# Optimization experiments

Hardware: AMD Instinct MI355X
Metric: run time of the kernel (lower is better)

Reference implementation:

```python
import jax, jax.numpy as jnp
import numpy as np

FEATS_DIM = 2048
NUM_CLASSES = 20
R_EASY, R_HARD = 5, 20
M_SMALL, M_BIG = 3, 6   # cfg.m, cfg.M (morphology structure widths)
N_HEADS = 4
B, T = 16, 750


def conv1d(x, w, b=None, pad=0):
    # x: [B, Cin, T], w: [Cout, Cin, K]
    out = jax.lax.conv_general_dilated(x, w, (1,), [(pad, pad)],
                                       dimension_numbers=('NCH', 'OIH', 'NCH'))
    return out if b is None else out + b[None, :, None]


def leaky(x):
    return jnp.where(x >= 0, x, 0.2 * x)


def mha(q, k, v, in_w, in_b, out_w, out_b):
    # torch nn.MultiheadAttention (batch_first, eval-mode: dropout off)
    Bq, Lq, E = q.shape
    Lk = k.shape[1]
    d = E // N_HEADS
    wq, wk, wv = jnp.split(in_w, 3, axis=0)
    bq, bk, bv = jnp.split(in_b, 3)
    qh = (q @ wq.T + bq).reshape(Bq, Lq, N_HEADS, d).transpose(0, 2, 1, 3)
    kh = (k @ wk.T + bk).reshape(Bq, Lk, N_HEADS, d).transpose(0, 2, 1, 3)
    vh = (v @ wv.T + bv).reshape(Bq, Lk, N_HEADS, d).transpose(0, 2, 1, 3)
    scores = jnp.einsum('bhqd,bhkd->bhqk', qh, kh) / jnp.sqrt(jnp.float32(d))
    attn = jax.nn.softmax(scores, axis=-1)
    o = jnp.einsum('bhqk,bhkd->bhqd', attn, vh).transpose(0, 2, 1, 3).reshape(Bq, Lq, E)
    return o @ out_w.T + out_b


def relational_head(x, P):
    # x: [B, 74, 2048] (the double transpose in the torch code cancels out)
    in1, in2 = x[:, :37], x[:, 37:]
    ao2 = mha(in1, in2, in2, P['in_w'], P['in_b'], P['out_w'], P['out_b'])
    ao1 = mha(in2, in1, in1, P['in_w'], P['in_b'], P['out_w'], P['out_b'])
    y = jnp.swapaxes(jnp.concatenate([ao1, ao2], axis=1), -1, -2)   # [B,2048,74]
    y = leaky(conv1d(y, P['c1_w'], P['c1_b'], pad=1))               # [B,128,74]
    y = leaky(conv1d(y, P['c2_w'], P['c2_b'], pad=1))               # [B,32,74]
    y = leaky(y @ P['l1_w'].T + P['l1_b'])                          # [B,32,10]
    y = y.reshape(y.shape[0], -1)                                   # [B,320]
    return jax.nn.sigmoid(y @ P['l2_w'].T + P['l2_b'])              # [B,1]


def select_topk(scores, emb, k):
    idx = jnp.argsort(-scores, axis=1)[:, :k]                       # descending
    return jnp.take_along_axis(emb, idx[:, :, None], axis=1)


def _morph(b, M, erosion):
    # scipy binary_erosion/dilation with structure ones((1,M)), border_value=0.
    # erosion: offsets [-M//2, M-1-M//2]; dilation (reflected): [-(M-1-M//2), M//2].
    Tn = b.shape[1]
    lo, hi = (M // 2, M - 1 - M // 2) if erosion else (M - 1 - M // 2, M // 2)
    pad = jnp.pad(b, ((0, 0), (lo, hi)))
    s = jnp.stack([pad[:, j:j + Tn] for j in range(M)], axis=0)
    return jnp.min(s, axis=0) if erosion else jnp.max(s, axis=0)


def cola_forward(x, P):
    # train=True path, eval-mode dropout (deterministic identity)
    Bn, Tn, _ = x.shape
    k_easy, k_hard = Tn // R_EASY, Tn // R_HARD
    feat = jnp.swapaxes(x, -1, -2)                                   # [B,2048,T]
    emb_c = jax.nn.relu(conv1d(feat, P['w_embed'], P['b_embed'], pad=1))
    embeddings = jnp.swapaxes(emb_c, -1, -2)                         # [B,T,2048]
    cas = jnp.swapaxes(jax.nn.relu(conv1d(emb_c, P['w_cls'], None)), -1, -2)  # [B,T,C]
    actionness = cas.sum(axis=-1)                                    # [B,T]
    a2 = jax.nn.relu(conv1d(actionness[:, None, :], P['tf1_w'], P['tf1_b'], pad=1))
    a2 = jax.nn.relu(conv1d(a2, P['tf2_w'], P['tf2_b'], pad=1))[:, 0]
    # easy snippet mining
    act_rev = actionness.max(axis=1, keepdims=True) - actionness
    easy_act = select_topk(actionness, embeddings, k_easy)
    easy_bkg = select_topk(act_rev, embeddings, k_easy)
    # hard snippet mining (binary morphology; indices are non-differentiable)
    a_det = jax.lax.stop_gradient(actionness)
    med = jnp.median(a_det, axis=1, keepdims=True)
    abin = jnp.where(a_det > med, 1.0, 0.0)
    inner = _morph(abin, M_SMALL, True) - _morph(abin, M_BIG, True)
    outer = _morph(abin, M_BIG, False) - _morph(abin, M_SMALL, False)
    hard_act = select_topk(actionness * inner, embeddings, k_hard)
    hard_bkg = select_topk(actionness * outer, embeddings, k_hard)
    split = lambda y: (y[:, :37], y[:, 37:74], y[:, 74:111], y[:, 111:148])
    ea0, ea1, ea2, ea3 = split(easy_act)
    eb0, eb1, eb2, eb3 = split(easy_bkg)
    rh = lambda a, b: relational_head(jnp.concatenate([a, b], axis=1), P)
    re_a_02 = rh(ea3, ea2); re_a_03 = rh(ea0, ea3); re_a_0h = rh(ea1, hard_act)
    re_b_02 = rh(eb3, eb2); re_b_03 = rh(eb0, eb3); re_b_0h = rh(eb1, hard_bkg)
    re_ab_23 = rh(ea2, eb3); re_ab_32 = rh(eb2, ea3); re_ab_33 = rh(ea3, eb3)
    re_ab_h3 = rh(hard_act, eb3); re_ab_3h = rh(ea3, hard_bkg); re_ab_hh = rh(hard_bkg, hard_act)
    video_scores = jax.nn.softmax((-jnp.sort(-cas, axis=1))[:, :k_easy].mean(axis=1), axis=1)
    return (video_scores, actionness, a2, cas,
            re_a_0h, re_a_02, re_a_03, re_b_0h, re_b_02, re_b_03,
            re_ab_hh, re_ab_3h, re_ab_h3, re_ab_33, re_ab_32, re_ab_23,
            easy_act, easy_bkg, hard_act, hard_bkg)


PARAM_NAMES = ['w_embed', 'b_embed', 'w_cls', 'tf1_w', 'tf1_b', 'tf2_w', 'tf2_b',
               'in_w', 'in_b', 'out_w', 'out_b', 'c1_w', 'c1_b', 'c2_w', 'c2_b',
               'l1_w', 'l1_b', 'l2_w', 'l2_b']


def setup_inputs() -> dict:
    key = jax.random.key(0)
    ks = jax.random.split(key, 20)
    sc = 0.02
    inp = {
        'x': jax.random.normal(ks[0], (B, T, FEATS_DIM), jnp.float32),
        'w_embed': sc * jax.random.normal(ks[1], (2048, FEATS_DIM, 3), jnp.float32),
        'b_embed': sc * jax.random.normal(ks[2], (2048,), jnp.float32),
        'w_cls': sc * jax.random.normal(ks[3], (NUM_CLASSES, 2048, 1), jnp.float32),
        'tf1_w': sc * jax.random.normal(ks[4], (1, 1, 3), jnp.float32),
        'tf1_b': sc * jax.random.normal(ks[5], (1,), jnp.float32),
        'tf2_w': sc * jax.random.normal(ks[6], (1, 1, 3), jnp.float32),
        'tf2_b': sc * jax.random.normal(ks[7], (1,), jnp.float32),
        'in_w': sc * jax.random.normal(ks[8], (3 * 2048, 2048), jnp.float32),
        'in_b': sc * jax.random.normal(ks[9], (3 * 2048,), jnp.float32),
        'out_w': sc * jax.random.normal(ks[10], (2048, 2048), jnp.float32),
        'out_b': sc * jax.random.normal(ks[11], (2048,), jnp.float32),
        'c1_w': sc * jax.random.normal(ks[12], (128, 2048, 3), jnp.float32),
        'c1_b': sc * jax.random.normal(ks[13], (128,), jnp.float32),
        'c2_w': sc * jax.random.normal(ks[14], (32, 128, 3), jnp.float32),
        'c2_b': sc * jax.random.normal(ks[15], (32,), jnp.float32),
        'l1_w': sc * jax.random.normal(ks[16], (10, 74), jnp.float32),
        'l1_b': sc * jax.random.normal(ks[17], (10,), jnp.float32),
        'l2_w': sc * jax.random.normal(ks[18], (1, 10 * 32), jnp.float32),
        'l2_b': sc * jax.random.normal(ks[19], (1,), jnp.float32),
    }
    return inp


def reference(x, w_embed, b_embed, w_cls, tf1_w, tf1_b, tf2_w, tf2_b,
              in_w, in_b, out_w, out_b, c1_w, c1_b, c2_w, c2_b,
              l1_w, l1_b, l2_w, l2_b):
    P = dict(w_embed=w_embed, b_embed=b_embed, w_cls=w_cls, tf1_w=tf1_w, tf1_b=tf1_b,
             tf2_w=tf2_w, tf2_b=tf2_b, in_w=in_w, in_b=in_b, out_w=out_w, out_b=out_b,
             c1_w=c1_w, c1_b=c1_b, c2_w=c2_w, c2_b=c2_b,
             l1_w=l1_w, l1_b=l1_b, l2_w=l2_w, l2_b=l2_b)
    return cola_forward(x, P)
```

## Files before the change

kernel.cpp:

```cpp
#include <hip/hip_runtime.h>


static __device__ __forceinline__ float leaky_f(float x) { return x >= 0.f ? x : 0.2f * x; }

typedef _Float16 f16;
typedef f16 f16x4 __attribute__((ext_vector_type(4)));
typedef f16 f16x8 __attribute__((ext_vector_type(8)));
typedef float f32x4 __attribute__((ext_vector_type(4)));

__device__ __constant__ int PIDX[12][2] = {
  {1, 8}, {3, 2}, {0, 3}, {5, 9}, {7, 6}, {4, 7},
  {9, 8}, {3, 9}, {8, 7}, {3, 7}, {6, 3}, {2, 7}};

__global__ __launch_bounds__(256) void pack_w_k(const float* __restrict__ src,
                                                float* __restrict__ dst,
                                                int N, int KC, int taps) {
  long total = (long)N * KC * taps;
  long i = (long)blockIdx.x * 256 + threadIdx.x;
  if (i >= total) return;
  long nk = (long)N * KC;
  int tap = (int)(i / nk);
  long rem = i - (long)tap * nk;
  int n = (int)(rem / KC);
  int k = (int)(rem - (long)n * KC);
  dst[i] = src[((long)n * KC + k) * taps + tap];
}

__global__ __launch_bounds__(256) void pack_frag_w_k(const float* __restrict__ src,
                                                     f16* __restrict__ dst,
                                                     int N, int KC, int taps) {
  int KCd32 = KC >> 5, gN = N >> 4;
  long total = (long)taps * KCd32 * gN * 512;
  long i = (long)blockIdx.x * 256 + threadIdx.x;
  if (i >= total) return;
  int e = (int)(i & 7);
  int lane = (int)((i >> 3) & 63);
  long rem = i >> 9;
  int g = (int)(rem % gN); rem /= gN;
  int kc = (int)(rem % KCd32);
  int tap = (int)(rem / KCd32);
  int n = g * 16 + (lane & 15);
  int k = kc * 32 + (lane >> 4) * 8 + e;
  float v = src[((long)n * KC + k) * taps + tap];
  f16 h = (f16)v;
  long f = ((long)tap * KCd32 + kc) * gN + g;
  dst[f * 1024 + lane * 8 + e] = h;
  dst[f * 1024 + 512 + lane * 8 + e] = (f16)(v - (float)h);
}

__global__ __launch_bounds__(256) void gemmf3_k(
    const float* __restrict__ A, const f16* __restrict__ Bf,
    const float* __restrict__ bias, float* __restrict__ C,
    int M, int N, int KC, int taps, int shift_base, int a_grp,
    int mblocks, int swz, int act) {
  __shared__ f16 Ah[128][40];
  __shared__ f16 Al[128][40];
  int t = threadIdx.x;
  int NB = gridDim.x;
  int linear = blockIdx.x;
  int wg = swz ? ((linear & 7) * (NB >> 3) + (linear >> 3)) : linear;
  int n0 = (wg / mblocks) * 128, m0 = (wg % mblocks) * 128;

  int sr = t >> 1;
  int sc = (t & 1) << 4;
  int am = m0 + sr;
  int ar = am % a_grp;

  int lane = t & 63, wv = t >> 6;
  int wm = (wv >> 1) * 64, wn = (wv & 1) * 64;
  int fr = lane & 15, fg = lane >> 4;

  int KCd32 = KC >> 5, gN = N >> 4;
  int g0 = ((n0 + wn) >> 4);

  f32x4 acc[4][4];
#pragma unroll
  for (int i = 0; i < 4; ++i)
#pragma unroll
    for (int j = 0; j < 4; ++j) acc[i][j] = (f32x4)(0.f);

  for (int tap = 0; tap < taps; ++tap) {
    int rr = ar + tap + shift_base;
    bool av = (am < M) && (rr >= 0) && (rr < a_grp);
    const float* ap = A + (long)(am + tap + shift_base) * KC + sc;
    long fb = ((long)tap * KCd32) * gN;
#pragma unroll 1
    for (int kc = 0; kc < KCd32; ++kc) {
      const f16* fp = Bf + (fb + (long)kc * gN + g0) * 1024 + lane * 8;
      f16x8 fbh[4], fbl[4];
#pragma unroll
      for (int j = 0; j < 4; ++j) {
        fbh[j] = *(const f16x8*)(fp + (long)j * 1024);
        fbl[j] = *(const f16x8*)(fp + (long)j * 1024 + 512);
      }
      float4 a4[4];
#pragma unroll
      for (int q = 0; q < 4; ++q)
        a4[q] = av ? *(const float4*)(ap + kc * 32 + q * 4)
                   : make_float4(0.f, 0.f, 0.f, 0.f);

      __syncthreads();
#pragma unroll
      for (int q = 0; q < 4; ++q) {
        float xs[4] = {a4[q].x, a4[q].y, a4[q].z, a4[q].w};
        f16x4 h4, l4;
#pragma unroll
        for (int e = 0; e < 4; ++e) {
          f16 hh = (f16)xs[e];
          h4[e] = hh;
          l4[e] = (f16)(xs[e] - (float)hh);
        }
        *(f16x4*)&Ah[sr][sc + q * 4] = h4;
        *(f16x4*)&Al[sr][sc + q * 4] = l4;
      }
      __syncthreads();

      f16x8 fah[4], fal[4];
#pragma unroll
      for (int i = 0; i < 4; ++i) {
        fah[i] = *(const f16x8*)&Ah[wm + i * 16 + fr][fg * 8];
        fal[i] = *(const f16x8*)&Al[wm + i * 16 + fr][fg * 8];
      }
#pragma unroll
      for (int i = 0; i < 4; ++i)
#pragma unroll
        for (int j = 0; j < 4; ++j) {
          acc[i][j] = __builtin_amdgcn_mfma_f32_16x16x32_f16(fal[i], fbh[j], acc[i][j], 0, 0, 0);
          acc[i][j] = __builtin_amdgcn_mfma_f32_16x16x32_f16(fah[i], fbl[j], acc[i][j], 0, 0, 0);
          acc[i][j] = __builtin_amdgcn_mfma_f32_16x16x32_f16(fah[i], fbh[j], acc[i][j], 0, 0, 0);
        }
    }
  }

#pragma unroll
  for (int i = 0; i < 4; ++i) {
#pragma unroll
    for (int j = 0; j < 4; ++j) {
      int col = n0 + wn + j * 16 + fr;
      if (col >= N) continue;
      float bb = bias ? bias[col] : 0.f;
#pragma unroll
      for (int r = 0; r < 4; ++r) {
        int m = m0 + wm + i * 16 + fg * 4 + r;
        if (m >= M) continue;
        float v = acc[i][j][r] + bb;
        if (act == 1) v = fmaxf(v, 0.f);
        else if (act == 2) v = leaky_f(v);
        C[(long)m * N + col] = v;
      }
    }
  }
}

template <int DACC>
__global__ __launch_bounds__(256) void gemm32_k(
    const float* __restrict__ A, const float* __restrict__ Bw,
    const float* __restrict__ bias, float* __restrict__ C,
    int M, int N, int KC, int taps, int shift_base,
    int a_grp, long a_bstride, int c_grp, long c_bstride, int act) {
  __shared__ __align__(16) float As[32][36];
  __shared__ __align__(16) float Bs[32][36];
  int tid = threadIdx.x;
  int n0 = blockIdx.x * 32, m0 = blockIdx.y * 32;
  int tx = tid & 15, ty = tid >> 4;
  int row_l = tid >> 3;
  int kq = (tid & 7) << 2;
  float accf[2][2] = {{0.f}};
  double accd[2][2];
  if (DACC) { accd[0][0] = accd[0][1] = accd[1][0] = accd[1][1] = 0.0; }
  int tpt = KC >> 5;
  int nkt = tpt * taps;
  int am = m0 + row_l;
  int agrp = 0, ar = 0;
  if (am < M) { agrp = am / a_grp; ar = am - agrp * a_grp; }
  int bn = n0 + row_l;
  for (int kt = 0; kt < nkt; ++kt) {
    int tap = kt / tpt;
    int k0 = (kt - tap * tpt) << 5;
    float4 av = make_float4(0.f, 0.f, 0.f, 0.f);
    float4 bv = make_float4(0.f, 0.f, 0.f, 0.f);
    if (am < M) {
      int rr = ar + tap + shift_base;
      if (rr >= 0 && rr < a_grp)
        av = *(const float4*)(A + (long)agrp * a_bstride + (long)rr * KC + (k0 + kq));
    }
    if (bn < N)
      bv = *(const float4*)(Bw + ((long)tap * N + bn) * KC + (k0 + kq));
    __syncthreads();
    As[kq + 0][row_l] = av.x; As[kq + 1][row_l] = av.y;
    As[kq + 2][row_l] = av.z; As[kq + 3][row_l] = av.w;
    Bs[kq + 0][row_l] = bv.x; Bs[kq + 1][row_l] = bv.y;
    Bs[kq + 2][row_l] = bv.z; Bs[kq + 3][row_l] = bv.w;
    __syncthreads();
    float tile[2][2] = {{0.f, 0.f}, {0.f, 0.f}};
#pragma unroll
    for (int k = 0; k < 32; ++k) {
      float2 a2 = *(const float2*)&As[k][ty << 1];
      float2 b2 = *(const float2*)&Bs[k][tx << 1];
      if (DACC) {
        tile[0][0] = fmaf(a2.x, b2.x, tile[0][0]);
        tile[0][1] = fmaf(a2.x, b2.y, tile[0][1]);
        tile[1][0] = fmaf(a2.y, b2.x, tile[1][0]);
        tile[1][1] = fmaf(a2.y, b2.y, tile[1][1]);
      } else {
        accf[0][0] = fmaf(a2.x, b2.x, accf[0][0]);
        accf[0][1] = fmaf(a2.x, b2.y, accf[0][1]);
        accf[1][0] = fmaf(a2.y, b2.x, accf[1][0]);
        accf[1][1] = fmaf(a2.y, b2.y, accf[1][1]);
      }
    }
    if (DACC) {
      accd[0][0] += (double)tile[0][0]; accd[0][1] += (double)tile[0][1];
      accd[1][0] += (double)tile[1][0]; accd[1][1] += (double)tile[1][1];
    }
  }
#pragma unroll
  for (int i = 0; i < 2; ++i) {
    int m = m0 + (ty << 1) + i;
    if (m >= M) continue;
    int grp = m / c_grp, r = m - grp * c_grp;
    float* crow = C + (long)grp * c_bstride + (long)r * N;
#pragma unroll
    for (int j = 0; j < 2; ++j) {
      int n = n0 + (tx << 1) + j;
      if (n >= N) continue;
      float v = DACC ? (float)accd[i][j] : accf[i][j];
      if (bias) v += bias[n];
      if (act == 1) v = fmaxf(v, 0.f);
      else if (act == 2) v = leaky_f(v);
      crow[n] = v;
    }
  }
}

template <int AMODE>
__global__ __launch_bounds__(256) void gemmx3_k(
    const float* __restrict__ Abase, const float* __restrict__ Bw,
    const float* __restrict__ bias, float* __restrict__ C,
    int M, int N, int K,
    long oEA, long oEB, long oHA, long oHB) {
  __shared__ _Float16 Ah[128][40];
  __shared__ _Float16 Al[128][40];
  __shared__ _Float16 Bh[128][40];
  __shared__ _Float16 Bl[128][40];
  int t = threadIdx.x;
  int m0 = blockIdx.y * 128, n0 = blockIdx.x * 128;

  int lr = t >> 3;
  int lq = t & 7;
  const float* arow[4];
  const float* brow[4];
#pragma unroll
  for (int p = 0; p < 4; ++p) {
    int m = m0 + p * 32 + lr;
    if (m < M) {
      if (AMODE == 0) {
        arow[p] = Abase + (long)m * K;
      } else {
        int inp = m / 592;
        int rem = m - inp * 592;
        int b = rem / 37;
        int r = rem - b * 37;
        long base, bstr;
        if (inp < 8) { base = (inp < 4 ? oEA : oEB) + (long)(inp & 3) * (37L * 2048); bstr = 150L * 2048; }
        else         { base = (inp == 8) ? oHA : oHB; bstr = 37L * 2048; }
        arow[p] = Abase + base + (long)b * bstr + (long)r * 2048;
      }
    } else arow[p] = nullptr;
    int n = n0 + p * 32 + lr;
    brow[p] = (n < N) ? (Bw + (long)n * K) : nullptr;
  }

  int lane = t & 63;
  int wv = t >> 6;
  int wm = (wv >> 1) * 64, wn = (wv & 1) * 64;
  int fr = lane & 15, fg = lane >> 4;

  f32x4 acc[4][4];
#pragma unroll
  for (int i = 0; i < 4; ++i)
#pragma unroll
    for (int j = 0; j < 4; ++j) acc[i][j] = (f32x4)(0.f);

  int nkt = K >> 5;
  for (int kt = 0; kt < nkt; ++kt) {
    int k0 = kt << 5;
    float4 av[4], bv[4];
#pragma unroll
    for (int p = 0; p < 4; ++p) {
      av[p] = arow[p] ? *(const float4*)(arow[p] + k0 + lq * 4) : make_float4(0.f, 0.f, 0.f, 0.f);
      bv[p] = brow[p] ? *(const float4*)(brow[p] + k0 + lq * 4) : make_float4(0.f, 0.f, 0.f, 0.f);
    }
    __syncthreads();
#pragma unroll
    for (int p = 0; p < 4; ++p) {
      int row = p * 32 + lr;
      float xs[4] = {av[p].x, av[p].y, av[p].z, av[p].w};
      f16x4 h, l;
#pragma unroll
      for (int e = 0; e < 4; ++e) {
        f16 hh = (f16)xs[e];
        h[e] = hh;
        l[e] = (f16)(xs[e] - (float)hh);
      }
      *(f16x4*)&Ah[row][lq * 4] = h;
      *(f16x4*)&Al[row][lq * 4] = l;
      float ys[4] = {bv[p].x, bv[p].y, bv[p].z, bv[p].w};
#pragma unroll
      for (int e = 0; e < 4; ++e) {
        f16 hh = (f16)ys[e];
        h[e] = hh;
        l[e] = (f16)(ys[e] - (float)hh);
      }
      *(f16x4*)&Bh[row][lq * 4] = h;
      *(f16x4*)&Bl[row][lq * 4] = l;
    }
    __syncthreads();
    f16x8 ah[4], alo[4], bh[4], blo[4];
#pragma unroll
    for (int i = 0; i < 4; ++i) {
      ah[i]  = *(const f16x8*)&Ah[wm + i * 16 + fr][fg * 8];
      alo[i] = *(const f16x8*)&Al[wm + i * 16 + fr][fg * 8];
      bh[i]  = *(const f16x8*)&Bh[wn + i * 16 + fr][fg * 8];
      blo[i] = *(const f16x8*)&Bl[wn + i * 16 + fr][fg * 8];
    }
#pragma unroll
    for (int i = 0; i < 4; ++i)
#pragma unroll
      for (int j = 0; j < 4; ++j) {
        acc[i][j] = __builtin_amdgcn_mfma_f32_16x16x32_f16(alo[i], bh[j], acc[i][j], 0, 0, 0);
        acc[i][j] = __builtin_amdgcn_mfma_f32_16x16x32_f16(ah[i], blo[j], acc[i][j], 0, 0, 0);
        acc[i][j] = __builtin_amdgcn_mfma_f32_16x16x32_f16(ah[i], bh[j], acc[i][j], 0, 0, 0);
      }
  }

#pragma unroll
  for (int i = 0; i < 4; ++i) {
#pragma unroll
    for (int j = 0; j < 4; ++j) {
      int col = n0 + wn + j * 16 + fr;
      if (col >= N) continue;
      float bb = bias ? bias[col] : 0.f;
#pragma unroll
      for (int r = 0; r < 4; ++r) {
        int m = m0 + wm + i * 16 + fg * 4 + r;
        if (m >= M) continue;
        C[(long)m * N + col] = acc[i][j][r] + bb;
      }
    }
  }
}

__global__ __launch_bounds__(256) void actionness_k(const float* __restrict__ cas,
                                                    float* __restrict__ act) {
  int p = blockIdx.x * 256 + threadIdx.x;
  if (p >= 16 * 750) return;
  double s = 0.0;
#pragma unroll
  for (int c = 0; c < 20; ++c) s += (double)cas[(long)p * 20 + c];
  act[p] = (float)s;
}

__global__ __launch_bounds__(256) void a2_k(const float* __restrict__ act,
                                            const float* __restrict__ tf1w, const float* __restrict__ tf1b,
                                            const float* __restrict__ tf2w, const float* __restrict__ tf2b,
                                            float* __restrict__ a2out) {
  __shared__ float s0[752];
  __shared__ float s1[752];
  int b = blockIdx.x, tid = threadIdx.x;
  for (int i = tid; i < 752; i += 256) { s0[i] = 0.f; s1[i] = 0.f; }
  __syncthreads();
  for (int t = tid; t < 750; t += 256) s0[t + 1] = act[b * 750 + t];
  __syncthreads();
  float w0 = tf1w[0], w1 = tf1w[1], w2 = tf1w[2], bb1 = tf1b[0];
  for (int t = tid; t < 750; t += 256)
    s1[t + 1] = fmaxf(w0 * s0[t] + w1 * s0[t + 1] + w2 * s0[t + 2] + bb1, 0.f);
  __syncthreads();
  float u0 = tf2w[0], u1 = tf2w[1], u2 = tf2w[2], bb2 = tf2b[0];
  for (int t = tid; t < 750; t += 256)
    a2out[b * 750 + t] = fmaxf(u0 * s1[t] + u1 * s1[t + 1] + u2 * s1[t + 2] + bb2, 0.f);
}

__global__ __launch_bounds__(256) void sort_topk_k(const float* __restrict__ scores,
                                                   int* __restrict__ out_idx, int K,
                                                   float* __restrict__ out_med,
                                                   float* __restrict__ out_mx) {
  __shared__ unsigned long long keys[1024];
  int b = blockIdx.x, tid = threadIdx.x;
  for (int i = tid; i < 1024; i += 256) {
    unsigned long long kv = 0ull;
    if (i < 750) {
      unsigned int bits = __float_as_uint(scores[b * 750 + i]);
      kv = ((unsigned long long)bits << 32) | (unsigned long long)(0xFFFFFFFFu - (unsigned)i);
    }
    keys[i] = kv;
  }
  __syncthreads();
  for (int k = 2; k <= 1024; k <<= 1) {
    for (int j = k >> 1; j > 0; j >>= 1) {
      for (int i = tid; i < 1024; i += 256) {
        int ixj = i ^ j;
        if (ixj > i) {
          unsigned long long a = keys[i], c = keys[ixj];
          bool sw = ((i & k) == 0) ? (a < c) : (a > c);
          if (sw) { keys[i] = c; keys[ixj] = a; }
        }
      }
      __syncthreads();
    }
  }
  for (int i = tid; i < K; i += 256)
    out_idx[b * K + i] = (int)(0xFFFFFFFFu - (unsigned int)(keys[i] & 0xFFFFFFFFull));
  if (tid == 0) {
    if (out_mx) out_mx[b] = __uint_as_float((unsigned int)(keys[0] >> 32));
    if (out_med) {
      float v1 = __uint_as_float((unsigned int)(keys[374] >> 32));
      float v2 = __uint_as_float((unsigned int)(keys[375] >> 32));
      out_med[b] = 0.5f * (v1 + v2);
    }
  }
}

__global__ __launch_bounds__(256) void morph_k(const float* __restrict__ act,
                                               const float* __restrict__ med,
                                               const float* __restrict__ mxv,
                                               float* __restrict__ arev,
                                               float* __restrict__ hsa,
                                               float* __restrict__ hsb) {
  __shared__ float ab[756];
  int b = blockIdx.x, tid = threadIdx.x;
  float m = med[b], M = mxv[b];
  for (int i = tid; i < 756; i += 256) ab[i] = 0.f;
  __syncthreads();
  for (int t = tid; t < 750; t += 256) {
    float a = act[b * 750 + t];
    ab[t + 3] = (a > m) ? 1.f : 0.f;
    arev[b * 750 + t] = M - a;
  }
  __syncthreads();
  for (int t = tid; t < 750; t += 256) {
    float e3 = fminf(ab[t + 2], fminf(ab[t + 3], ab[t + 4]));
    float e6 = fminf(fminf(ab[t], ab[t + 1]),
                     fminf(fminf(ab[t + 2], ab[t + 3]), fminf(ab[t + 4], ab[t + 5])));
    float d3 = fmaxf(ab[t + 2], fmaxf(ab[t + 3], ab[t + 4]));
    float d6 = fmaxf(fmaxf(ab[t + 1], ab[t + 2]),
                     fmaxf(fmaxf(ab[t + 3], ab[t + 4]), fmaxf(ab[t + 5], ab[t + 6])));
    float a = act[b * 750 + t];
    hsa[b * 750 + t] = a * (e3 - e6);
    hsb[b * 750 + t] = a * (d6 - d3);
  }
}

__global__ __launch_bounds__(256) void gather_k(const float* __restrict__ emb,
                                                const int* __restrict__ idx,
                                                float* __restrict__ dst, int K) {
  int blk = blockIdx.x;
  int b = blk / K, i = blk - b * K;
  int t = idx[b * K + i];
  const float4* src = (const float4*)(emb + ((long)(b * 750 + t)) * 2048);
  float4* d = (float4*)(dst + (long)blk * 2048);
  for (int u = threadIdx.x; u < 512; u += 256) d[u] = src[u];
}

__global__ __launch_bounds__(256) void vtop_k(const float* __restrict__ cas,
                                              float* __restrict__ s) {
  __shared__ float v[1024];
  int b = blockIdx.x / 20, c = blockIdx.x - b * 20;
  int tid = threadIdx.x;
  for (int i = tid; i < 1024; i += 256)
    v[i] = (i < 750) ? cas[((long)(b * 750 + i)) * 20 + c] : -1.f;
  __syncthreads();
  for (int k = 2; k <= 1024; k <<= 1) {
    for (int j = k >> 1; j > 0; j >>= 1) {
      for (int i = tid; i < 1024; i += 256) {
        int ixj = i ^ j;
        if (ixj > i) {
          float a = v[i], cc = v[ixj];
          bool sw = ((i & k) == 0) ? (a < cc) : (a > cc);
          if (sw) { v[i] = cc; v[ixj] = a; }
        }
      }
      __syncthreads();
    }
  }
  if (tid == 0) {
    float sum = 0.f;
    for (int i = 0; i < 150; ++i) sum += v[i];
    s[b * 20 + c] = sum / 150.f;
  }
}

__global__ __launch_bounds__(64) void softmax20_k(const float* __restrict__ s,
                                                  float* __restrict__ out) {
  int b = blockIdx.x;
  if (threadIdx.x != 0) return;
  float mx = -3.4e38f;
  for (int c = 0; c < 20; ++c) mx = fmaxf(mx, s[b * 20 + c]);
  float e[20]; float sum = 0.f;
  for (int c = 0; c < 20; ++c) { e[c] = expf(s[b * 20 + c] - mx); sum += e[c]; }
  for (int c = 0; c < 20; ++c) out[b * 20 + c] = e[c] / sum;
}

__global__ __launch_bounds__(64) void attn_scores_k(const float* __restrict__ q10,
                                                    int head0,
                                                    float* __restrict__ attnb) {
  int hl = blockIdx.y >> 1, call = blockIdx.y & 1;
  int head = head0 + hl;
  int iA = PIDX[head][0], iB = PIDX[head][1];
  const float* q  = q10 + (long)(call ? iA : iB) * 592 * 6144;
  const float* kv = q10 + (long)(call ? iB : iA) * 592 * 6144;
  int x = blockIdx.x;
  int b = x / 148; int rem = x - b * 148; int h = rem / 37; int qi = rem - h * 37;
  int lane = threadIdx.x;
  const float scale = 0.04419417382415922f;
  const float* qp = q + ((long)(b * 37 + qi)) * 6144 + h * 512;
  float qr[8];
#pragma unroll
  for (int j = 0; j < 8; ++j) qr[j] = qp[lane + 64 * j] * scale;
  __shared__ float sc[37];
  for (int ki = 0; ki < 37; ++ki) {
    const float* kp = kv + ((long)(b * 37 + ki)) * 6144 + 2048 + h * 512;
    float d = 0.f;
#pragma unroll
    for (int j = 0; j < 8; ++j) d = fmaf(qr[j], kp[lane + 64 * j], d);
    for (int off = 32; off > 0; off >>= 1) d += __shfl_down(d, off, 64);
    if (lane == 0) sc[ki] = d;
  }
  __syncthreads();
  float v = (lane < 37) ? sc[lane] : -3.4e38f;
  float mx = v;
  for (int off = 32; off > 0; off >>= 1) mx = fmaxf(mx, __shfl_xor(mx, off, 64));
  float e = (lane < 37) ? expf(v - mx) : 0.f;
  float sum = e;
  for (int off = 32; off > 0; off >>= 1) sum += __shfl_xor(sum, off, 64);
  if (lane < 37)
    attnb[(((long)(((hl * 2 + call) * 16 + b) * 4 + h)) * 37 + qi) * 37 + lane] = e / sum;
}

__global__ __launch_bounds__(256) void attn_v_k(const float* __restrict__ q10,
                                                int head0,
                                                const float* __restrict__ attnb,
                                                float* __restrict__ obuf) {
  int hl = blockIdx.y >> 1, call = blockIdx.y & 1;
  int head = head0 + hl;
  int iA = PIDX[head][0], iB = PIDX[head][1];
  const float* kv = q10 + (long)(call ? iB : iA) * 592 * 6144;
  int x = blockIdx.x;
  int b = x / 37, qi = x - b * 37;
  int tid = threadIdx.x;
  __shared__ float at[4][37];
  if (tid < 148) {
    int h = tid / 37, ki = tid - h * 37;
    at[h][ki] = attnb[(((long)(((hl * 2 + call) * 16 + b) * 4 + h)) * 37 + qi) * 37 + ki];
  }
  __syncthreads();
  int yoff = call ? 37 : 0;
  float* op = obuf + (long)hl * (16L * 74 * 2048) + ((long)(b * 74 + yoff + qi)) * 2048;
#pragma unroll
  for (int i = 0; i < 8; ++i) {
    int c = tid + 256 * i;
    int h = c >> 9;
    float acc = 0.f;
#pragma unroll 1
    for (int ki = 0; ki < 37; ++ki)
      acc = fmaf(at[h][ki], kv[((long)(b * 37 + ki)) * 6144 + 4096 + c], acc);
    op[c] = acc;
  }
}

__global__ __launch_bounds__(320) void head_tail_k(const float* __restrict__ c2o,
                                                   const float* __restrict__ l1w,
                                                   const float* __restrict__ l1b,
                                                   const float* __restrict__ l2w,
                                                   const float* __restrict__ l2b,
                                                   float* __restrict__ out) {
  __shared__ float h[320];
  int blk = blockIdx.x, tid = threadIdx.x;
  int c = tid / 10, j = tid - c * 10;
  float acc = l1b[j];
  for (int l = 0; l < 74; ++l)
    acc = fmaf(c2o[((long)(blk * 74 + l)) * 32 + c], l1w[j * 74 + l], acc);
  acc = leaky_f(acc);
  h[c * 10 + j] = acc * l2w[c * 10 + j];
  __syncthreads();
  if (tid == 0) {
    float s = l2b[0];
    for (int i = 0; i < 320; ++i) s += h[i];
    out[blk] = 1.f / (1.f + expf(-s));
  }
}

extern "C" void kernel_launch(void* const* d_in, const int* in_sizes, int n_in,
                              void* d_out, int out_size, void* d_ws, size_t ws_size,
                              hipStream_t stream) {
  const float* x       = (const float*)d_in[0];
  const float* w_embed = (const float*)d_in[1];
  const float* b_embed = (const float*)d_in[2];
  const float* w_cls   = (const float*)d_in[3];
  const float* tf1_w   = (const float*)d_in[4];
  const float* tf1_b   = (const float*)d_in[5];
  const float* tf2_w   = (const float*)d_in[6];
  const float* tf2_b   = (const float*)d_in[7];
  const float* in_w    = (const float*)d_in[8];
  const float* in_b    = (const float*)d_in[9];
  const float* out_w   = (const float*)d_in[10];
  const float* out_b   = (const float*)d_in[11];
  const float* c1_w    = (const float*)d_in[12];
  const float* c1_b    = (const float*)d_in[13];
  const float* c2_w    = (const float*)d_in[14];
  const float* c2_b    = (const float*)d_in[15];
  const float* l1_w    = (const float*)d_in[16];
  const float* l1_b    = (const float*)d_in[17];
  const float* l2_w    = (const float*)d_in[18];
  const float* l2_b    = (const float*)d_in[19];
  float* out = (float*)d_out;
  float* ws  = (float*)d_ws;

  const long O_VS = 0, O_ACT = 320, O_A2 = 12320, O_CAS = 24320, O_RH = 264320;
  const long O_EA = 264512;
  const long O_EB = O_EA + 16L * 150 * 2048;
  const long O_HA = O_EB + 16L * 150 * 2048;
  const long O_HB = O_HA + 16L * 37 * 2048;

  long o = 0;
  float* emb   = ws + o; o += 12000L * 2048;
  f16*   embWf = (f16*)(ws + o); o += 12582912;
  float* q10   = ws;
  f16*   c1Wf  = (f16*)(ws + o); o += 786432;
  float* wpk2  = ws + o; o += 3L * 32 * 128;
  float* arev  = ws + o; o += 12000;
  float* hsa   = ws + o; o += 12000;
  float* hsb   = ws + o; o += 12000;
  float* med   = ws + o; o += 16;
  float* mxv   = ws + o; o += 16;
  float* vsbuf = ws + o; o += 320;
  int* idxEA = (int*)(ws + o); o += 2400;
  int* idxEB = (int*)(ws + o); o += 2400;
  int* idxHA = (int*)(ws + o); o += 592;
  int* idxHB = (int*)(ws + o); o += 592;
  long oTail = o;
  (void)in_sizes; (void)n_in; (void)out_size;

  const long SZ_ATTNB12 = 12L * 2 * 16 * 4 * 37 * 37;
  const long SZ_OBUF12  = 12L * 16 * 74 * 2048;
  const long SZ_C1O12   = 14208L * 128;
  const long SZ_C2O12   = 14208L * 32;
  long needB = oTail + SZ_ATTNB12 + SZ_OBUF12 + SZ_C1O12 + SZ_C2O12;
  bool batched = (ws_size >= (size_t)needB * 4);

  pack_frag_w_k<<<(12582912 + 255) / 256, 256, 0, stream>>>(w_embed, embWf, 2048, 2048, 3);
  pack_frag_w_k<<<(786432 + 255) / 256, 256, 0, stream>>>(c1_w, c1Wf, 128, 2048, 3);
  pack_w_k<<<(12288 + 255) / 256, 256, 0, stream>>>(c2_w, wpk2, 32, 128, 3);

  gemmf3_k<<<1504, 256, 0, stream>>>(x, embWf, b_embed, emb,
      12000, 2048, 2048, 3, -1, 750, 94, 1, 1);

  gemm32_k<1><<<dim3(1, 375), 256, 0, stream>>>(emb, w_cls, nullptr, out + O_CAS,
      12000, 20, 2048, 1, 0, 750, 1536000L, 750, 15000L, 1);

  actionness_k<<<47, 256, 0, stream>>>(out + O_CAS, out + O_ACT);
  a2_k<<<16, 256, 0, stream>>>(out + O_ACT, tf1_w, tf1_b, tf2_w, tf2_b, out + O_A2);

  vtop_k<<<320, 256, 0, stream>>>(out + O_CAS, vsbuf);
  softmax20_k<<<16, 64, 0, stream>>>(vsbuf, out + O_VS);

  sort_topk_k<<<16, 256, 0, stream>>>(out + O_ACT, idxEA, 150, med, mxv);
  morph_k<<<16, 256, 0, stream>>>(out + O_ACT, med, mxv, arev, hsa, hsb);
  sort_topk_k<<<16, 256, 0, stream>>>(arev, idxEB, 150, nullptr, nullptr);
  sort_topk_k<<<16, 256, 0, stream>>>(hsa, idxHA, 37, nullptr, nullptr);
  sort_topk_k<<<16, 256, 0, stream>>>(hsb, idxHB, 37, nullptr, nullptr);

  gather_k<<<2400, 256, 0, stream>>>(emb, idxEA, out + O_EA, 150);
  gather_k<<<2400, 256, 0, stream>>>(emb, idxEB, out + O_EB, 150);
  gather_k<<<592, 256, 0, stream>>>(emb, idxHA, out + O_HA, 37);
  gather_k<<<592, 256, 0, stream>>>(emb, idxHB, out + O_HB, 37);

  gemmx3_k<1><<<dim3(48, 47), 256, 0, stream>>>(out, in_w, in_b, q10,
      5920, 6144, 2048, O_EA, O_EB, O_HA, O_HB);

  if (batched) {
    float* attnbB = ws + oTail;
    float* obufB  = attnbB + SZ_ATTNB12;
    float* c1oB   = obufB + SZ_OBUF12;
    float* c2oB   = c1oB + SZ_C1O12;
    float* ybufB  = ws;

    attn_scores_k<<<dim3(2368, 24), 64, 0, stream>>>(q10, 0, attnbB);
    attn_v_k<<<dim3(592, 24), 256, 0, stream>>>(q10, 0, attnbB, obufB);
    gemmx3_k<0><<<dim3(16, 111), 256, 0, stream>>>(obufB, out_w, out_b, ybufB,
        14208, 2048, 2048, 0, 0, 0, 0);
    gemmf3_k<<<111, 256, 0, stream>>>(ybufB, c1Wf, c1_b, c1oB,
        14208, 128, 2048, 3, -1, 74, 111, 0, 2);
    gemm32_k<0><<<dim3(1, 444), 256, 0, stream>>>(c1oB, wpk2, c2_b, c2oB,
        14208, 32, 128, 3, -1, 74, 74L * 128, 74, 74L * 32, 2);
    head_tail_k<<<192, 320, 0, stream>>>(c2oB, l1_w, l1_b, l2_w, l2_b, out + O_RH);
  } else {
    float* attnbL = ws + oTail;
    float* obufL  = attnbL + 2L * 16 * 4 * 37 * 37;
    float* ybufL  = obufL + 16L * 74 * 2048;
    float* c1oL   = ybufL + 16L * 74 * 2048;
    float* c2oL   = c1oL + 1184L * 128;
    for (int i = 0; i < 12; ++i) {
      attn_scores_k<<<dim3(2368, 2), 64, 0, stream>>>(q10, i, attnbL);
      attn_v_k<<<dim3(592, 2), 256, 0, stream>>>(q10, i, attnbL, obufL);
      gemmx3_k<0><<<dim3(16, 10), 256, 0, stream>>>(obufL, out_w, out_b, ybufL,
          1184, 2048, 2048, 0, 0, 0, 0);
      gemmf3_k<<<10, 256, 0, stream>>>(ybufL, c1Wf, c1_b, c1oL,
          1184, 128, 2048, 3, -1, 74, 10, 0, 2);
      gemm32_k<0><<<dim3(1, 37), 256, 0, stream>>>(c1oL, wpk2, c2_b, c2oL,
          1184, 32, 128, 3, -1, 74, 74L * 128, 74, 74L * 32, 2);
      head_tail_k<<<16, 320, 0, stream>>>(c2oL, l1_w, l1_b, l2_w, l2_b, out + O_RH + 16L * i);
    }
  }
}
```

Measured before the change: 3.446 ms.

## Double-buffer split-f16 GEMM and batch sort, gather and attention kernels

The split-precision MFMA GEMM now keeps two LDS buffers and flattens the tap/k loops, so the next A tile is prefetched from global memory while the current one is consumed, with one barrier per step instead of two. The three top-k sorts are merged into a single launch, and the four gathers into another, to cut launch overhead. The attention score kernel now gives each 256-thread block all 37 queries of one (batch, head) pair, and attn_v processes eight queries per block so each V load is reused across them. The cost is doubled LDS for the GEMM and fewer, larger blocks for the attention kernels, which may lower parallelism.

New measurement: 2.862 ms. -17.0%, faster.

```diff
diff --git a/kernel.cpp b/kernel.cpp
--- a/kernel.cpp
+++ b/kernel.cpp
@@ -53,25 +53,26 @@
     const float* __restrict__ bias, float* __restrict__ C,
     int M, int N, int KC, int taps, int shift_base, int a_grp,
     int mblocks, int swz, int act) {
-  __shared__ f16 Ah[128][40];
-  __shared__ f16 Al[128][40];
+  __shared__ f16 Ah[2][128][40];
+  __shared__ f16 Al[2][128][40];
   int t = threadIdx.x;
   int NB = gridDim.x;
   int linear = blockIdx.x;
   int wg = swz ? ((linear & 7) * (NB >> 3) + (linear >> 3)) : linear;
   int n0 = (wg / mblocks) * 128, m0 = (wg % mblocks) * 128;
 
-  int sr = t >> 1;
-  int sc = (t & 1) << 4;
+  int sr = t >> 1, sc = (t & 1) << 4;
   int am = m0 + sr;
   int ar = am % a_grp;
+  const float* rbase = A + (long)am * KC;
 
   int lane = t & 63, wv = t >> 6;
   int wm = (wv >> 1) * 64, wn = (wv & 1) * 64;
   int fr = lane & 15, fg = lane >> 4;
 
   int KCd32 = KC >> 5, gN = N >> 4;
-  int g0 = ((n0 + wn) >> 4);
+  int g0 = (n0 + wn) >> 4;
+  int nkt = taps * KCd32;
 
   f32x4 acc[4][4];
 #pragma unroll
@@ -79,57 +80,64 @@
 #pragma unroll
     for (int j = 0; j < 4; ++j) acc[i][j] = (f32x4)(0.f);
 
-  for (int tap = 0; tap < taps; ++tap) {
+  auto loada = [&](int kt, float4* a4) {
+    int tap = kt / KCd32;
+    int kc = kt - tap * KCd32;
     int rr = ar + tap + shift_base;
     bool av = (am < M) && (rr >= 0) && (rr < a_grp);
-    const float* ap = A + (long)(am + tap + shift_base) * KC + sc;
-    long fb = ((long)tap * KCd32) * gN;
+    const float* ap = rbase + (long)(tap + shift_base) * KC + (kc << 5) + sc;
+#pragma unroll
+    for (int q = 0; q < 4; ++q)
+      a4[q] = av ? *(const float4*)(ap + q * 4) : make_float4(0.f, 0.f, 0.f, 0.f);
+  };
+  auto storea = [&](int buf, const float4* a4) {
+#pragma unroll
+    for (int q = 0; q < 4; ++q) {
+      float xs[4] = {a4[q].x, a4[q].y, a4[q].z, a4[q].w};
+      f16x4 h4, l4;
+#pragma unroll
+      for (int e = 0; e < 4; ++e) {
+        f16 hh = (f16)xs[e];
+        h4[e] = hh;
+        l4[e] = (f16)(xs[e] - (float)hh);
+      }
+      *(f16x4*)&Ah[buf][sr][sc + q * 4] = h4;
+      *(f16x4*)&Al[buf][sr][sc + q * 4] = l4;
+    }
+  };
+
+  float4 a4[4];
+  loada(0, a4);
+  storea(0, a4);
+
 #pragma unroll 1
-    for (int kc = 0; kc < KCd32; ++kc) {
-      const f16* fp = Bf + (fb + (long)kc * gN + g0) * 1024 + lane * 8;
-      f16x8 fbh[4], fbl[4];
+  for (int kt = 0; kt < nkt; ++kt) {
+    int buf = kt & 1;
+    const f16* fp = Bf + ((long)kt * gN + g0) * 1024 + lane * 8;
+    f16x8 fbh[4], fbl[4];
+#pragma unroll
+    for (int j = 0; j < 4; ++j) {
+      fbh[j] = *(const f16x8*)(fp + (long)j * 1024);
+      fbl[j] = *(const f16x8*)(fp + (long)j * 1024 + 512);
+    }
+    bool havn = (kt + 1 < nkt);
+    if (havn) loada(kt + 1, a4);
+    __syncthreads();
+    f16x8 fah[4], fal[4];
+#pragma unroll
+    for (int i = 0; i < 4; ++i) {
+      fah[i] = *(const f16x8*)&Ah[buf][wm + i * 16 + fr][fg * 8];
+      fal[i] = *(const f16x8*)&Al[buf][wm + i * 16 + fr][fg * 8];
+    }
+    if (havn) storea(buf ^ 1, a4);
+#pragma unroll
+    for (int i = 0; i < 4; ++i)
 #pragma unroll
       for (int j = 0; j < 4; ++j) {
-        fbh[j] = *(const f16x8*)(fp + (long)j * 1024);
-        fbl[j] = *(const f16x8*)(fp + (long)j * 1024 + 512);
-      }
-      float4 a4[4];
-#pragma unroll
-      for (int q = 0; q < 4; ++q)
-        a4[q] = av ? *(const float4*)(ap + kc * 32 + q * 4)
-                   : make_float4(0.f, 0.f, 0.f, 0.f);
-
-      __syncthreads();
-#pragma unroll
-      for (int q = 0; q < 4; ++q) {
-        float xs[4] = {a4[q].x, a4[q].y, a4[q].z, a4[q].w};
-        f16x4 h4, l4;
-#pragma unroll
-        for (int e = 0; e < 4; ++e) {
-          f16 hh = (f16)xs[e];
-          h4[e] = hh;
-          l4[e] = (f16)(xs[e] - (float)hh);
-        }
-        *(f16x4*)&Ah[sr][sc + q * 4] = h4;
-        *(f16x4*)&Al[sr][sc + q * 4] = l4;
-      }
-      __syncthreads();
-
-      f16x8 fah[4], fal[4];
-#pragma unroll
-      for (int i = 0; i < 4; ++i) {
-        fah[i] = *(const f16x8*)&Ah[wm + i * 16 + fr][fg * 8];
-        fal[i] = *(const f16x8*)&Al[wm + i * 16 + fr][fg * 8];
-      }
-#pragma unroll
-      for (int i = 0; i < 4; ++i)
-#pragma unroll
-        for (int j = 0; j < 4; ++j) {
-          acc[i][j] = __builtin_amdgcn_mfma_f32_16x16x32_f16(fal[i], fbh[j], acc[i][j], 0, 0, 0);
-          acc[i][j] = __builtin_amdgcn_mfma_f32_16x16x32_f16(fah[i], fbl[j], acc[i][j], 0, 0, 0);
-          acc[i][j] = __builtin_amdgcn_mfma_f32_16x16x32_f16(fah[i], fbh[j], acc[i][j], 0, 0, 0);
-        }
-    }
+        acc[i][j] = __builtin_amdgcn_mfma_f32_16x16x32_f16(fal[i], fbh[j], acc[i][j], 0, 0, 0);
+        acc[i][j] = __builtin_amdgcn_mfma_f32_16x16x32_f16(fah[i], fbl[j], acc[i][j], 0, 0, 0);
+        acc[i][j] = __builtin_amdgcn_mfma_f32_16x16x32_f16(fah[i], fbh[j], acc[i][j], 0, 0, 0);
+      }
   }
 
 #pragma unroll
@@ -421,6 +429,44 @@
   }
 }
 
+__global__ __launch_bounds__(256) void sort3_k(const float* __restrict__ arev,
+                                               const float* __restrict__ hsa,
+                                               const float* __restrict__ hsb,
+                                               int* __restrict__ idxEB,
+                                               int* __restrict__ idxHA,
+                                               int* __restrict__ idxHB) {
+  __shared__ unsigned long long keys[1024];
+  int which = blockIdx.x >> 4;
+  int b = blockIdx.x & 15, tid = threadIdx.x;
+  const float* s = (which == 0) ? arev : (which == 1) ? hsa : hsb;
+  int* oi = (which == 0) ? idxEB : (which == 1) ? idxHA : idxHB;
+  int K = (which == 0) ? 150 : 37;
+  for (int i = tid; i < 1024; i += 256) {
+    unsigned long long kv = 0ull;
+    if (i < 750) {
+      unsigned int bits = __float_as_uint(s[b * 750 + i]);
+      kv = ((unsigned long long)bits << 32) | (unsigned long long)(0xFFFFFFFFu - (unsigned)i);
+    }
+    keys[i] = kv;
+  }
+  __syncthreads();
+  for (int k = 2; k <= 1024; k <<= 1) {
+    for (int j = k >> 1; j > 0; j >>= 1) {
+      for (int i = tid; i < 1024; i += 256) {
+        int ixj = i ^ j;
+        if (ixj > i) {
+          unsigned long long a = keys[i], c = keys[ixj];
+          bool sw = ((i & k) == 0) ? (a < c) : (a > c);
+          if (sw) { keys[i] = c; keys[ixj] = a; }
+        }
+      }
+      __syncthreads();
+    }
+  }
+  for (int i = tid; i < K; i += 256)
+    oi[b * K + i] = (int)(0xFFFFFFFFu - (unsigned int)(keys[i] & 0xFFFFFFFFull));
+}
+
 __global__ __launch_bounds__(256) void morph_k(const float* __restrict__ act,
                                                const float* __restrict__ med,
                                                const float* __restrict__ mxv,
@@ -451,14 +497,25 @@
   }
 }
 
-__global__ __launch_bounds__(256) void gather_k(const float* __restrict__ emb,
-                                                const int* __restrict__ idx,
-                                                float* __restrict__ dst, int K) {
+__global__ __launch_bounds__(256) void gather4_k(const float* __restrict__ emb,
+                                                 const int* __restrict__ idxEA,
+                                                 const int* __restrict__ idxEB,
+                                                 const int* __restrict__ idxHA,
+                                                 const int* __restrict__ idxHB,
+                                                 float* __restrict__ dEA,
+                                                 float* __restrict__ dEB,
+                                                 float* __restrict__ dHA,
+                                                 float* __restrict__ dHB) {
   int blk = blockIdx.x;
-  int b = blk / K, i = blk - b * K;
-  int t = idx[b * K + i];
+  const int* idx; float* dst; int K, rel;
+  if (blk < 2400)      { idx = idxEA; dst = dEA; K = 150; rel = blk; }
+  else if (blk < 4800) { idx = idxEB; dst = dEB; K = 150; rel = blk - 2400; }
+  else if (blk < 5392) { idx = idxHA; dst = dHA; K = 37;  rel = blk - 4800; }
+  else                 { idx = idxHB; dst = dHB; K = 37;  rel = blk - 5392; }
+  int b = rel / K;
+  int t = idx[rel];
   const float4* src = (const float4*)(emb + ((long)(b * 750 + t)) * 2048);
-  float4* d = (float4*)(dst + (long)blk * 2048);
+  float4* d = (float4*)(dst + (long)rel * 2048);
   for (int u = threadIdx.x; u < 512; u += 256) d[u] = src[u];
 }
 
@@ -501,40 +558,42 @@
   for (int c = 0; c < 20; ++c) out[b * 20 + c] = e[c] / sum;
 }
 
-__global__ __launch_bounds__(64) void attn_scores_k(const float* __restrict__ q10,
-                                                    int head0,
-                                                    float* __restrict__ attnb) {
+__global__ __launch_bounds__(256) void attn_scores_k(const float* __restrict__ q10,
+                                                     int head0,
+                                                     float* __restrict__ attnb) {
   int hl = blockIdx.y >> 1, call = blockIdx.y & 1;
   int head = head0 + hl;
   int iA = PIDX[head][0], iB = PIDX[head][1];
   const float* q  = q10 + (long)(call ? iA : iB) * 592 * 6144;
   const float* kv = q10 + (long)(call ? iB : iA) * 592 * 6144;
-  int x = blockIdx.x;
-  int b = x / 148; int rem = x - b * 148; int h = rem / 37; int qi = rem - h * 37;
-  int lane = threadIdx.x;
+  int b = blockIdx.x >> 2, h = blockIdx.x & 3;
+  int wv = threadIdx.x >> 6, lane = threadIdx.x & 63;
+  __shared__ float sc[4][37];
   const float scale = 0.04419417382415922f;
-  const float* qp = q + ((long)(b * 37 + qi)) * 6144 + h * 512;
-  float qr[8];
-#pragma unroll
-  for (int j = 0; j < 8; ++j) qr[j] = qp[lane + 64 * j] * scale;
-  __shared__ float sc[37];
-  for (int ki = 0; ki < 37; ++ki) {
-    const float* kp = kv + ((long)(b * 37 + ki)) * 6144 + 2048 + h * 512;
-    float d = 0.f;
-#pragma unroll
-    for (int j = 0; j < 8; ++j) d = fmaf(qr[j], kp[lane + 64 * j], d);
-    for (int off = 32; off > 0; off >>= 1) d += __shfl_down(d, off, 64);
-    if (lane == 0) sc[ki] = d;
-  }
-  __syncthreads();
-  float v = (lane < 37) ? sc[lane] : -3.4e38f;
-  float mx = v;
-  for (int off = 32; off > 0; off >>= 1) mx = fmaxf(mx, __shfl_xor(mx, off, 64));
-  float e = (lane < 37) ? expf(v - mx) : 0.f;
-  float sum = e;
-  for (int off = 32; off > 0; off >>= 1) sum += __shfl_xor(sum, off, 64);
-  if (lane < 37)
-    attnb[(((long)(((hl * 2 + call) * 16 + b) * 4 + h)) * 37 + qi) * 37 + lane] = e / sum;
+  const float* kbase = kv + ((long)(b * 37)) * 6144 + 2048 + h * 512;
+  long outbase = (((long)(((hl * 2 + call) * 16 + b) * 4 + h)) * 37) * 37;
+  for (int qi = wv; qi < 37; qi += 4) {
+    const float* qp = q + ((long)(b * 37 + qi)) * 6144 + h * 512;
+    float qr[8];
+#pragma unroll
+    for (int j = 0; j < 8; ++j) qr[j] = qp[lane + 64 * j] * scale;
+    for (int ki = 0; ki < 37; ++ki) {
+      const float* kp = kbase + (long)ki * 6144;
+      float d = 0.f;
+#pragma unroll
+      for (int j = 0; j < 8; ++j) d = fmaf(qr[j], kp[lane + 64 * j], d);
+      for (int off = 32; off > 0; off >>= 1) d += __shfl_down(d, off, 64);
+      if (lane == 0) sc[wv][ki] = d;
+    }
+    float v = (lane < 37) ? sc[wv][lane] : -3.4e38f;
+    float mx = v;
+    for (int off = 32; off > 0; off >>= 1) mx = fmaxf(mx, __shfl_xor(mx, off, 64));
+    float e = (lane < 37) ? expf(v - mx) : 0.f;
+    float sum = e;
+    for (int off = 32; off > 0; off >>= 1) sum += __shfl_xor(sum, off, 64);
+    if (lane < 37)
+      attnb[outbase + (long)qi * 37 + lane] = e / sum;
+  }
 }
 
 __global__ __launch_bounds__(256) void attn_v_k(const float* __restrict__ q10,
@@ -545,26 +604,47 @@
   int head = head0 + hl;
   int iA = PIDX[head][0], iB = PIDX[head][1];
   const float* kv = q10 + (long)(call ? iB : iA) * 592 * 6144;
-  int x = blockIdx.x;
-  int b = x / 37, qi = x - b * 37;
+  int b = blockIdx.x / 5, qg = blockIdx.x - b * 5;
   int tid = threadIdx.x;
-  __shared__ float at[4][37];
-  if (tid < 148) {
-    int h = tid / 37, ki = tid - h * 37;
-    at[h][ki] = attnb[(((long)(((hl * 2 + call) * 16 + b) * 4 + h)) * 37 + qi) * 37 + ki];
+  __shared__ float at[4][37][8];
+  long abase = ((long)(((hl * 2 + call) * 16 + b) * 4)) * 37 * 37;
+  for (int idx = tid; idx < 4 * 37 * 8; idx += 256) {
+    int q = idx & 7;
+    int ki = (idx >> 3) % 37;
+    int h = idx / (37 * 8);
+    int qi = qg * 8 + q;
+    float v = 0.f;
+    if (qi < 37) v = attnb[abase + ((long)h * 37 + qi) * 37 + ki];
+    at[h][ki][q] = v;
   }
   __syncthreads();
   int yoff = call ? 37 : 0;
-  float* op = obuf + (long)hl * (16L * 74 * 2048) + ((long)(b * 74 + yoff + qi)) * 2048;
-#pragma unroll
+  const float* vbase = kv + ((long)(b * 37)) * 6144 + 4096;
+  float* obase = obuf + (long)hl * (16L * 74 * 2048) + ((long)(b * 74 + yoff)) * 2048;
+#pragma unroll 1
   for (int i = 0; i < 8; ++i) {
     int c = tid + 256 * i;
     int h = c >> 9;
-    float acc = 0.f;
+    float acc[8] = {0.f, 0.f, 0.f, 0.f, 0.f, 0.f, 0.f, 0.f};
 #pragma unroll 1
-    for (int ki = 0; ki < 37; ++ki)
-      acc = fmaf(at[h][ki], kv[((long)(b * 37 + ki)) * 6144 + 4096 + c], acc);
-    op[c] = acc;
+    for (int ki = 0; ki < 37; ++ki) {
+      float vv = vbase[(long)ki * 6144 + c];
+      float4 a0 = *(const float4*)&at[h][ki][0];
+      float4 a1 = *(const float4*)&at[h][ki][4];
+      acc[0] = fmaf(a0.x, vv, acc[0]);
+      acc[1] = fmaf(a0.y, vv, acc[1]);
+      acc[2] = fmaf(a0.z, vv, acc[2]);
+      acc[3] = fmaf(a0.w, vv, acc[3]);
+      acc[4] = fmaf(a1.x, vv, acc[4]);
+      acc[5] = fmaf(a1.y, vv, acc[5]);
+      acc[6] = fmaf(a1.z, vv, acc[6]);
+      acc[7] = fmaf(a1.w, vv, acc[7]);
+    }
+#pragma unroll
+    for (int q = 0; q < 8; ++q) {
+      int qi = qg * 8 + q;
+      if (qi < 37) obase[(long)qi * 2048 + c] = acc[q];
+    }
   }
 }
 
@@ -666,14 +746,9 @@
 
   sort_topk_k<<<16, 256, 0, stream>>>(out + O_ACT, idxEA, 150, med, mxv);
   morph_k<<<16, 256, 0, stream>>>(out + O_ACT, med, mxv, arev, hsa, hsb);
-  sort_topk_k<<<16, 256, 0, stream>>>(arev, idxEB, 150, nullptr, nullptr);
-  sort_topk_k<<<16, 256, 0, stream>>>(hsa, idxHA, 37, nullptr, nullptr);
-  sort_topk_k<<<16, 256, 0, stream>>>(hsb, idxHB, 37, nullptr, nullptr);
-
-  gather_k<<<2400, 256, 0, stream>>>(emb, idxEA, out + O_EA, 150);
-  gather_k<<<2400, 256, 0, stream>>>(emb, idxEB, out + O_EB, 150);
-  gather_k<<<592, 256, 0, stream>>>(emb, idxHA, out + O_HA, 37);
-  gather_k<<<592, 256, 0, stream>>>(emb, idxHB, out + O_HB, 37);
+  sort3_k<<<48, 256, 0, stream>>>(arev, hsa, hsb, idxEB, idxHA, idxHB);
+  gather4_k<<<5984, 256, 0, stream>>>(emb, idxEA, idxEB, idxHA, idxHB,
+      out + O_EA, out + O_EB, out + O_HA, out + O_HB);
 
   gemmx3_k<1><<<dim3(48, 47), 256, 0, stream>>>(out, in_w, in_b, q10,
       5920, 6144, 2048, O_EA, O_EB, O_HA, O_HB);
@@ -685,8 +760,8 @@
     float* c2oB   = c1oB + SZ_C1O12;
     float* ybufB  = ws;
 
-    attn_scores_k<<<dim3(2368, 24), 64, 0, stream>>>(q10, 0, attnbB);
-    attn_v_k<<<dim3(592, 24), 256, 0, stream>>>(q10, 0, attnbB, obufB);
+    attn_scores_k<<<dim3(64, 24), 256, 0, stream>>>(q10, 0, attnbB);
+    attn_v_k<<<dim3(80, 24), 256, 0, stream>>>(q10, 0, attnbB, obufB);
     gemmx3_k<0><<<dim3(16, 111), 256, 0, stream>>>(obufB, out_w, out_b, ybufB,
         14208, 2048, 2048, 0, 0, 0, 0);
     gemmf3_k<<<111, 256, 0, stream>>>(ybufB, c1Wf, c1_b, c1oB,
@@ -701,8 +776,8 @@
     float* c1oL   = ybufL + 16L * 74 * 2048;
     float* c2oL   = c1oL + 1184L * 128;
     for (int i = 0; i < 12; ++i) {
-      attn_scores_k<<<dim3(2368, 2), 64, 0, stream>>>(q10, i, attnbL);
-      attn_v_k<<<dim3(592, 2), 256, 0, stream>>>(q10, i, attnbL, obufL);
+      attn_scores_k<<<dim3(64, 2), 256, 0, stream>>>(q10, i, attnbL);
+      attn_v_k<<<dim3(80, 2), 256, 0, stream>>>(q10, i, attnbL, obufL);
       gemmx3_k<0><<<dim3(16, 10), 256, 0, stream>>>(obufL, out_w, out_b, ybufL,
           1184, 2048, 2048, 0, 0, 0, 0);
       gemmf3_k<<<10, 256, 0, stream>>>(ybufL, c1Wf, c1_b, c1oL,
```
